# Optimization experiments

Hardware: AMD Instinct MI355X
Metric: run time of the kernel (lower is better)

## Reference

```python
import jax, jax.numpy as jnp
import numpy as np

B, N, DIM = 8, 1024, 1024
HEADS, DIM_HEAD = 16, 64
INNER = HEADS * DIM_HEAD  # 1024


def setup_inputs() -> dict:
    key = jax.random.key(0)
    k1, k2, k3 = jax.random.split(key, 3)
    x = jax.random.normal(k1, (B, N, DIM), dtype=jnp.float32)
    # Dense kernels (Glorot-ish scale for numerical sanity)
    w_qkv = jax.random.normal(k2, (DIM, 3 * INNER), dtype=jnp.float32) * (DIM ** -0.5)
    w_out = jax.random.normal(k3, (INNER, DIM), dtype=jnp.float32) * (INNER ** -0.5)
    b_out = jnp.zeros((DIM,), dtype=jnp.float32)
    return {"x": x, "w_qkv": w_qkv, "w_out": w_out, "b_out": b_out}


def reference(x, w_qkv, w_out, b_out):
    scale = DIM_HEAD ** -0.5
    qkv = x @ w_qkv                                   # [B, N, 3*INNER]
    q, k, v = jnp.split(qkv, 3, axis=-1)              # each [B, N, INNER]

    def to_heads(t):
        # [B, N, H*Dh] -> [B, H, N, Dh]
        return t.reshape(B, N, HEADS, DIM_HEAD).transpose(0, 2, 1, 3)

    q, k, v = to_heads(q), to_heads(k), to_heads(v)
    dots = jnp.einsum("bhid,bhjd->bhij", q, k) * scale   # [B, H, N, N]
    attn = jax.nn.softmax(dots, axis=-1)
    out = jnp.einsum("bhij,bhjd->bhid", attn, v)          # [B, H, N, Dh]
    out = out.transpose(0, 2, 1, 3).reshape(B, N, INNER)  # merge heads
    return out @ w_out + b_out                            # project_out (dropout inactive at inference)
```

## Files before the change

kernel.cpp:

```cpp
#include <hip/hip_runtime.h>
#include <hip/hip_bf16.h>
#include <math.h>

typedef __bf16 bf16_t;
typedef __bf16 bf16x4 __attribute__((ext_vector_type(4)));
typedef __bf16 bf16x8 __attribute__((ext_vector_type(8)));
typedef float f32x4 __attribute__((ext_vector_type(4)));

#define LOG2E 1.44269504088896340736f

#define GL2LDS(g, l)                                                     \
  __builtin_amdgcn_global_load_lds(                                      \
      (const __attribute__((address_space(1))) unsigned int*)(g),        \
      (__attribute__((address_space(3))) unsigned int*)(l), 16, 0, 0)

__global__ __launch_bounds__(256) void convert_f32_bf16(const float* __restrict__ in,
                                                        bf16_t* __restrict__ out) {
  const size_t idx = (size_t)(blockIdx.x * 256 + threadIdx.x) * 8;
  f32x4 a = *(const f32x4*)&in[idx];
  f32x4 b = *(const f32x4*)&in[idx + 4];
  bf16x8 v;
#pragma unroll
  for (int i = 0; i < 4; i++) { v[i] = (bf16_t)a[i]; v[i + 4] = (bf16_t)b[i]; }
  *(bf16x8*)&out[idx] = v;
}

__global__ __launch_bounds__(256) void transpose_f32_bf16(const float* __restrict__ in,
                                                          bf16_t* __restrict__ out,
                                                          int R, int C) {
  __shared__ bf16_t t[64][65];
  const int c0 = blockIdx.x * 64, r0 = blockIdx.y * 64;
  const int tx = threadIdx.x, ty = threadIdx.y;
#pragma unroll
  for (int i = 0; i < 16; i++) {
    int r = ty + i * 4;
    t[r][tx] = (bf16_t)in[(size_t)(r0 + r) * C + c0 + tx];
  }
  __syncthreads();
#pragma unroll
  for (int i = 0; i < 16; i++) {
    int r = ty + i * 4;
    out[(size_t)(c0 + r) * R + r0 + tx] = t[tx][r];
  }
}

template <int MODE>
__global__ __launch_bounds__(256) void gemm128(const bf16_t* __restrict__ A,
                                               const bf16_t* __restrict__ Bt,
                                               bf16_t* __restrict__ Qb,
                                               bf16_t* __restrict__ Kb,
                                               bf16_t* __restrict__ Vtb,
                                               const float* __restrict__ bias,
                                               float* __restrict__ Out) {
  constexpr int K = 1024;
  __shared__ __align__(16) bf16_t As[128 * 64];
  __shared__ __align__(16) bf16_t Bs[128 * 64];
  const int m0 = blockIdx.y * 128, n0 = blockIdx.x * 128;
  const int tid = threadIdx.x;
  const int w = tid >> 6, l = tid & 63;
  const int lr = l & 15, lq = l >> 4;
  const int lrx = lr & 7;
  const int wm = (w & 1) * 64, wn = (w >> 1) * 64;
  const int sR[4] = {(0 * 256 + tid) >> 3, (1 * 256 + tid) >> 3,
                     (2 * 256 + tid) >> 3, (3 * 256 + tid) >> 3};
  int sC[4];
#pragma unroll
  for (int i = 0; i < 4; i++) sC[i] = ((tid & 7) ^ (sR[i] & 7)) * 8;
  f32x4 acc[4][4] = {};

  for (int k0 = 0; k0 < K; k0 += 64) {
#pragma unroll
    for (int i = 0; i < 4; i++) {
      const int ldsoff = (i * 256 + w * 64) * 8;
      GL2LDS(&A[(size_t)(m0 + sR[i]) * K + k0 + sC[i]], &As[ldsoff]);
      GL2LDS(&Bt[(size_t)(n0 + sR[i]) * K + k0 + sC[i]], &Bs[ldsoff]);
    }
    __syncthreads();
#pragma unroll
    for (int ks = 0; ks < 2; ks++) {
      const int g = ks * 4 + lq;
      const int sw = ((g ^ lrx) << 3);
      bf16x8 af[4], bfr[4];
#pragma unroll
      for (int mt = 0; mt < 4; mt++)
        af[mt] = *(const bf16x8*)&As[((wm + mt * 16 + lr) << 6) + sw];
#pragma unroll
      for (int nt = 0; nt < 4; nt++)
        bfr[nt] = *(const bf16x8*)&Bs[((wn + nt * 16 + lr) << 6) + sw];
#pragma unroll
      for (int mt = 0; mt < 4; mt++)
#pragma unroll
        for (int nt = 0; nt < 4; nt++)
          acc[mt][nt] = __builtin_amdgcn_mfma_f32_16x16x32_bf16(af[mt], bfr[nt],
                                                                acc[mt][nt], 0, 0, 0);
    }
    __syncthreads();
  }

#pragma unroll
  for (int mt = 0; mt < 4; mt++)
#pragma unroll
    for (int nt = 0; nt < 4; nt++)
#pragma unroll
      for (int i = 0; i < 4; i++) {
        int m = m0 + wm + mt * 16 + lq * 4 + i;
        int c = n0 + wn + nt * 16 + lr;
        float v = acc[mt][nt][i];
        if (MODE == 1) {
          Out[(size_t)m * 1024 + c] = v + bias[c];
        } else {
          int b = m >> 10, n = m & 1023;
          int which = c >> 10, cc = c & 1023;
          int hh = cc >> 6, d = cc & 63;
          size_t qk = ((size_t)((b * 16 + hh) * 1024 + n)) * 64 + d;
          if (which == 0)
            Qb[qk] = (bf16_t)(v * (0.125f * LOG2E));
          else if (which == 1)
            Kb[qk] = (bf16_t)v;
          else
            Vtb[((size_t)((b * 16 + hh) * 64 + d)) * 1024 + n] = (bf16_t)v;
        }
      }
}

#define KVS 68
#define PS  72
__global__ __launch_bounds__(256) void attn128(const bf16_t* __restrict__ Qb,
                                               const bf16_t* __restrict__ Kb,
                                               const bf16_t* __restrict__ Vtb,
                                               bf16_t* __restrict__ Ob) {
  __shared__ __align__(16) bf16_t Ks[2][64 * KVS];
  __shared__ __align__(16) bf16_t Vs[2][64 * KVS];
  __shared__ __align__(16) bf16_t Pl[4 * 32 * PS];
  const int bid = blockIdx.x;
  const int qt = bid & 7, h = (bid >> 3) & 15, b = bid >> 7;
  const bf16_t* Qh = Qb + (size_t)((b * 16 + h) * 1024) * 64;
  const bf16_t* Kh = Kb + (size_t)((b * 16 + h) * 1024) * 64;
  const bf16_t* Vh = Vtb + (size_t)((b * 16 + h) * 64) * 1024;
  const int tid = threadIdx.x, w = tid >> 6, l = tid & 63;
  const int lr = l & 15, lq = l >> 4;
  const int q0 = qt * 128 + w * 32;

  bf16x8 onesf;
#pragma unroll
  for (int i = 0; i < 8; i++) onesf[i] = (lr == 0) ? (bf16_t)1.0f : (bf16_t)0.0f;

  const int sr = tid >> 3, sc = tid & 7;

  bf16x8 qf[2][2];
#pragma unroll
  for (int mt = 0; mt < 2; mt++)
#pragma unroll
    for (int ks = 0; ks < 2; ks++)
      qf[mt][ks] = *(const bf16x8*)&Qh[(size_t)(q0 + mt * 16 + lr) * 64 + ks * 32 + lq * 8];

  {
    bf16x8 k0 = *(const bf16x8*)&Kh[(size_t)sr * 64 + sc * 8];
    bf16x8 k1 = *(const bf16x8*)&Kh[(size_t)(sr + 32) * 64 + sc * 8];
    bf16x8 v0 = *(const bf16x8*)&Vh[(size_t)sr * 1024 + sc * 8];
    bf16x8 v1 = *(const bf16x8*)&Vh[(size_t)(sr + 32) * 1024 + sc * 8];
    *(bf16x8*)&Ks[0][sr * KVS + sc * 8] = k0;
    *(bf16x8*)&Ks[0][(sr + 32) * KVS + sc * 8] = k1;
    *(bf16x8*)&Vs[0][sr * KVS + sc * 8] = v0;
    *(bf16x8*)&Vs[0][(sr + 32) * KVS + sc * 8] = v1;
  }
  __syncthreads();

  f32x4 o[2][4] = {};
  f32x4 o5[2] = {};
  bf16_t* pw = &Pl[w * 32 * PS];

  for (int it = 0; it < 16; ++it) {
    const int buf = it & 1;
    bf16x8 nk0, nk1, nv0, nv1;
    if (it < 15) {
      const int jn = (it + 1) * 64;
      nk0 = *(const bf16x8*)&Kh[(size_t)(jn + sr) * 64 + sc * 8];
      nk1 = *(const bf16x8*)&Kh[(size_t)(jn + sr + 32) * 64 + sc * 8];
      nv0 = *(const bf16x8*)&Vh[(size_t)sr * 1024 + jn + sc * 8];
      nv1 = *(const bf16x8*)&Vh[(size_t)(sr + 32) * 1024 + jn + sc * 8];
    }
    f32x4 s[2][4] = {};
#pragma unroll
    for (int ks = 0; ks < 2; ks++)
#pragma unroll
      for (int nt = 0; nt < 4; nt++) {
        bf16x8 kf = *(const bf16x8*)&Ks[buf][(nt * 16 + lr) * KVS + ks * 32 + lq * 8];
#pragma unroll
        for (int mt = 0; mt < 2; mt++)
          s[mt][nt] = __builtin_amdgcn_mfma_f32_16x16x32_bf16(qf[mt][ks], kf, s[mt][nt], 0, 0, 0);
      }
#pragma unroll
    for (int mt = 0; mt < 2; mt++)
#pragma unroll
      for (int nt = 0; nt < 4; nt++)
#pragma unroll
        for (int i = 0; i < 4; i++)
          pw[(mt * 16 + lq * 4 + i) * PS + nt * 16 + lr] = (bf16_t)exp2f(s[mt][nt][i]);
#pragma unroll
    for (int ks = 0; ks < 2; ks++) {
      bf16x8 af[2];
#pragma unroll
      for (int mt = 0; mt < 2; mt++)
        af[mt] = *(const bf16x8*)&pw[(mt * 16 + lr) * PS + ks * 32 + lq * 8];
#pragma unroll
      for (int nt = 0; nt < 4; nt++) {
        bf16x8 vf = *(const bf16x8*)&Vs[buf][(nt * 16 + lr) * KVS + ks * 32 + lq * 8];
#pragma unroll
        for (int mt = 0; mt < 2; mt++)
          o[mt][nt] = __builtin_amdgcn_mfma_f32_16x16x32_bf16(af[mt], vf, o[mt][nt], 0, 0, 0);
      }
#pragma unroll
      for (int mt = 0; mt < 2; mt++)
        o5[mt] = __builtin_amdgcn_mfma_f32_16x16x32_bf16(af[mt], onesf, o5[mt], 0, 0, 0);
    }
    if (it < 15) {
      *(bf16x8*)&Ks[buf ^ 1][sr * KVS + sc * 8] = nk0;
      *(bf16x8*)&Ks[buf ^ 1][(sr + 32) * KVS + sc * 8] = nk1;
      *(bf16x8*)&Vs[buf ^ 1][sr * KVS + sc * 8] = nv0;
      *(bf16x8*)&Vs[buf ^ 1][(sr + 32) * KVS + sc * 8] = nv1;
    }
    __syncthreads();
  }
#pragma unroll
  for (int mt = 0; mt < 2; mt++)
#pragma unroll
    for (int i = 0; i < 4; i++) {
      float lsum = __shfl(o5[mt][i], lq * 16);
      float inv = 1.0f / lsum;
      int grow = b * 1024 + q0 + mt * 16 + lq * 4 + i;
#pragma unroll
      for (int nt = 0; nt < 4; nt++) {
        int col = h * 64 + nt * 16 + lr;
        Ob[(size_t)grow * 1024 + col] = (bf16_t)(o[mt][nt][i] * inv);
      }
    }
}

extern "C" void kernel_launch(void* const* d_in, const int* in_sizes, int n_in,
                              void* d_out, int out_size, void* d_ws, size_t ws_size,
                              hipStream_t stream) {
  const float* x     = (const float*)d_in[0];
  const float* w_qkv = (const float*)d_in[1];
  const float* w_out = (const float*)d_in[2];
  const float* b_out = (const float*)d_in[3];
  float* out = (float*)d_out;

  bf16_t* ws = (bf16_t*)d_ws;
  const size_t SZ = (size_t)8 * 1024 * 1024;
  bf16_t* Qb  = ws;
  bf16_t* Kb  = Qb + SZ;
  bf16_t* Vtb = Kb + SZ;
  bf16_t* Ob  = Vtb + SZ;
  bf16_t* Wqt = Ob + SZ;
  bf16_t* Wot = Wqt + (size_t)3072 * 1024;
  bf16_t* Xb  = Ob;

  hipLaunchKernelGGL(convert_f32_bf16, dim3(4096), dim3(256), 0, stream, x, Xb);
  hipLaunchKernelGGL(transpose_f32_bf16, dim3(48, 16), dim3(64, 4), 0, stream,
                     w_qkv, Wqt, 1024, 3072);
  hipLaunchKernelGGL(transpose_f32_bf16, dim3(16, 16), dim3(64, 4), 0, stream,
                     w_out, Wot, 1024, 1024);
  hipLaunchKernelGGL((gemm128<0>), dim3(24, 64), dim3(256), 0, stream,
                     Xb, Wqt, Qb, Kb, Vtb, (const float*)nullptr, (float*)nullptr);
  hipLaunchKernelGGL(attn128, dim3(1024), dim3(256), 0, stream, Qb, Kb, Vtb, Ob);
  hipLaunchKernelGGL((gemm128<1>), dim3(8, 64), dim3(256), 0, stream,
                     Ob, Wot, (bf16_t*)nullptr, (bf16_t*)nullptr, (bf16_t*)nullptr,
                     b_out, out);
}
```

Measured before the change: 282.2 us.

## Async direct-to-LDS K/V loads with XOR swizzle in attention; narrower out-proj tiles

The attention kernel now loads K and V tiles with global_load_lds straight into an XOR-swizzled unpadded LDS layout. This replaces the register staging and the separate LDS store phase, so the next tile's copy overlaps compute without holding registers. Block indexing is reordered so the query tile is the slowest-varying index, and the P scratch pitch changes. The output projection GEMM uses a 128x64 tile, doubling its grid to 1024 blocks for better CU occupancy, at the cost of less reuse per block.

After: 323.5 us. +14.6%, slower.

```diff
diff --git a/kernel.cpp b/kernel.cpp
--- a/kernel.cpp
+++ b/kernel.cpp
@@ -44,7 +44,7 @@
   }
 }
 
-template <int MODE>
+template <int MODE, int BN>
 __global__ __launch_bounds__(256) void gemm128(const bf16_t* __restrict__ A,
                                                const bf16_t* __restrict__ Bt,
                                                bf16_t* __restrict__ Qb,
@@ -53,26 +53,33 @@
                                                const float* __restrict__ bias,
                                                float* __restrict__ Out) {
   constexpr int K = 1024;
+  constexpr int NT = BN / 32;
+  constexpr int NB = BN / 32;
   __shared__ __align__(16) bf16_t As[128 * 64];
-  __shared__ __align__(16) bf16_t Bs[128 * 64];
-  const int m0 = blockIdx.y * 128, n0 = blockIdx.x * 128;
+  __shared__ __align__(16) bf16_t Bs[BN * 64];
+  const int m0 = blockIdx.y * 128, n0 = blockIdx.x * BN;
   const int tid = threadIdx.x;
   const int w = tid >> 6, l = tid & 63;
   const int lr = l & 15, lq = l >> 4;
   const int lrx = lr & 7;
-  const int wm = (w & 1) * 64, wn = (w >> 1) * 64;
-  const int sR[4] = {(0 * 256 + tid) >> 3, (1 * 256 + tid) >> 3,
-                     (2 * 256 + tid) >> 3, (3 * 256 + tid) >> 3};
-  int sC[4];
-#pragma unroll
-  for (int i = 0; i < 4; i++) sC[i] = ((tid & 7) ^ (sR[i] & 7)) * 8;
-  f32x4 acc[4][4] = {};
+  const int wm = (w & 1) * 64, wn = (w >> 1) * (BN / 2);
+  int sR[4], sC[4];
+#pragma unroll
+  for (int i = 0; i < 4; i++) {
+    sR[i] = (i * 256 + tid) >> 3;
+    sC[i] = ((tid & 7) ^ (sR[i] & 7)) * 8;
+  }
+  f32x4 acc[4][NT] = {};
 
   for (int k0 = 0; k0 < K; k0 += 64) {
 #pragma unroll
     for (int i = 0; i < 4; i++) {
       const int ldsoff = (i * 256 + w * 64) * 8;
       GL2LDS(&A[(size_t)(m0 + sR[i]) * K + k0 + sC[i]], &As[ldsoff]);
+    }
+#pragma unroll
+    for (int i = 0; i < NB; i++) {
+      const int ldsoff = (i * 256 + w * 64) * 8;
       GL2LDS(&Bt[(size_t)(n0 + sR[i]) * K + k0 + sC[i]], &Bs[ldsoff]);
     }
     __syncthreads();
@@ -80,17 +87,17 @@
     for (int ks = 0; ks < 2; ks++) {
       const int g = ks * 4 + lq;
       const int sw = ((g ^ lrx) << 3);
-      bf16x8 af[4], bfr[4];
+      bf16x8 af[4], bfr[NT];
 #pragma unroll
       for (int mt = 0; mt < 4; mt++)
         af[mt] = *(const bf16x8*)&As[((wm + mt * 16 + lr) << 6) + sw];
 #pragma unroll
-      for (int nt = 0; nt < 4; nt++)
+      for (int nt = 0; nt < NT; nt++)
         bfr[nt] = *(const bf16x8*)&Bs[((wn + nt * 16 + lr) << 6) + sw];
 #pragma unroll
       for (int mt = 0; mt < 4; mt++)
 #pragma unroll
-        for (int nt = 0; nt < 4; nt++)
+        for (int nt = 0; nt < NT; nt++)
           acc[mt][nt] = __builtin_amdgcn_mfma_f32_16x16x32_bf16(af[mt], bfr[nt],
                                                                 acc[mt][nt], 0, 0, 0);
     }
@@ -100,7 +107,7 @@
 #pragma unroll
   for (int mt = 0; mt < 4; mt++)
 #pragma unroll
-    for (int nt = 0; nt < 4; nt++)
+    for (int nt = 0; nt < NT; nt++)
 #pragma unroll
       for (int i = 0; i < 4; i++) {
         int m = m0 + wm + mt * 16 + lq * 4 + i;
@@ -123,29 +130,33 @@
       }
 }
 
-#define KVS 68
-#define PS  72
+#define PS 76
 __global__ __launch_bounds__(256) void attn128(const bf16_t* __restrict__ Qb,
                                                const bf16_t* __restrict__ Kb,
                                                const bf16_t* __restrict__ Vtb,
                                                bf16_t* __restrict__ Ob) {
-  __shared__ __align__(16) bf16_t Ks[2][64 * KVS];
-  __shared__ __align__(16) bf16_t Vs[2][64 * KVS];
+  __shared__ __align__(16) bf16_t Ks[2][64 * 64];
+  __shared__ __align__(16) bf16_t Vs[2][64 * 64];
   __shared__ __align__(16) bf16_t Pl[4 * 32 * PS];
   const int bid = blockIdx.x;
-  const int qt = bid & 7, h = (bid >> 3) & 15, b = bid >> 7;
+  const int qt = bid >> 7, idx = bid & 127;
+  const int h = idx & 15, b = idx >> 4;
   const bf16_t* Qh = Qb + (size_t)((b * 16 + h) * 1024) * 64;
   const bf16_t* Kh = Kb + (size_t)((b * 16 + h) * 1024) * 64;
   const bf16_t* Vh = Vtb + (size_t)((b * 16 + h) * 64) * 1024;
   const int tid = threadIdx.x, w = tid >> 6, l = tid & 63;
   const int lr = l & 15, lq = l >> 4;
+  const int lrx = lr & 7;
   const int q0 = qt * 128 + w * 32;
 
   bf16x8 onesf;
 #pragma unroll
   for (int i = 0; i < 8; i++) onesf[i] = (lr == 0) ? (bf16_t)1.0f : (bf16_t)0.0f;
 
-  const int sr = tid >> 3, sc = tid & 7;
+  const int sr = tid >> 3;
+  const int scc = ((tid & 7) ^ (sr & 7)) * 8;
+  const int ldsA = w * 512;
+  const int ldsB = 2048 + w * 512;
 
   bf16x8 qf[2][2];
 #pragma unroll
@@ -154,16 +165,10 @@
     for (int ks = 0; ks < 2; ks++)
       qf[mt][ks] = *(const bf16x8*)&Qh[(size_t)(q0 + mt * 16 + lr) * 64 + ks * 32 + lq * 8];
 
-  {
-    bf16x8 k0 = *(const bf16x8*)&Kh[(size_t)sr * 64 + sc * 8];
-    bf16x8 k1 = *(const bf16x8*)&Kh[(size_t)(sr + 32) * 64 + sc * 8];
-    bf16x8 v0 = *(const bf16x8*)&Vh[(size_t)sr * 1024 + sc * 8];
-    bf16x8 v1 = *(const bf16x8*)&Vh[(size_t)(sr + 32) * 1024 + sc * 8];
-    *(bf16x8*)&Ks[0][sr * KVS + sc * 8] = k0;
-    *(bf16x8*)&Ks[0][(sr + 32) * KVS + sc * 8] = k1;
-    *(bf16x8*)&Vs[0][sr * KVS + sc * 8] = v0;
-    *(bf16x8*)&Vs[0][(sr + 32) * KVS + sc * 8] = v1;
-  }
+  GL2LDS(&Kh[(size_t)sr * 64 + scc], &Ks[0][ldsA]);
+  GL2LDS(&Kh[(size_t)(sr + 32) * 64 + scc], &Ks[0][ldsB]);
+  GL2LDS(&Vh[(size_t)sr * 1024 + scc], &Vs[0][ldsA]);
+  GL2LDS(&Vh[(size_t)(sr + 32) * 1024 + scc], &Vs[0][ldsB]);
   __syncthreads();
 
   f32x4 o[2][4] = {};
@@ -172,24 +177,25 @@
 
   for (int it = 0; it < 16; ++it) {
     const int buf = it & 1;
-    bf16x8 nk0, nk1, nv0, nv1;
     if (it < 15) {
       const int jn = (it + 1) * 64;
-      nk0 = *(const bf16x8*)&Kh[(size_t)(jn + sr) * 64 + sc * 8];
-      nk1 = *(const bf16x8*)&Kh[(size_t)(jn + sr + 32) * 64 + sc * 8];
-      nv0 = *(const bf16x8*)&Vh[(size_t)sr * 1024 + jn + sc * 8];
-      nv1 = *(const bf16x8*)&Vh[(size_t)(sr + 32) * 1024 + jn + sc * 8];
+      GL2LDS(&Kh[(size_t)(jn + sr) * 64 + scc], &Ks[buf ^ 1][ldsA]);
+      GL2LDS(&Kh[(size_t)(jn + sr + 32) * 64 + scc], &Ks[buf ^ 1][ldsB]);
+      GL2LDS(&Vh[(size_t)sr * 1024 + jn + scc], &Vs[buf ^ 1][ldsA]);
+      GL2LDS(&Vh[(size_t)(sr + 32) * 1024 + jn + scc], &Vs[buf ^ 1][ldsB]);
     }
     f32x4 s[2][4] = {};
 #pragma unroll
-    for (int ks = 0; ks < 2; ks++)
+    for (int ks = 0; ks < 2; ks++) {
+      const int sw = (((ks * 4 + lq) ^ lrx) << 3);
 #pragma unroll
       for (int nt = 0; nt < 4; nt++) {
-        bf16x8 kf = *(const bf16x8*)&Ks[buf][(nt * 16 + lr) * KVS + ks * 32 + lq * 8];
+        bf16x8 kf = *(const bf16x8*)&Ks[buf][((nt * 16 + lr) << 6) + sw];
 #pragma unroll
         for (int mt = 0; mt < 2; mt++)
           s[mt][nt] = __builtin_amdgcn_mfma_f32_16x16x32_bf16(qf[mt][ks], kf, s[mt][nt], 0, 0, 0);
       }
+    }
 #pragma unroll
     for (int mt = 0; mt < 2; mt++)
 #pragma unroll
@@ -199,13 +205,14 @@
           pw[(mt * 16 + lq * 4 + i) * PS + nt * 16 + lr] = (bf16_t)exp2f(s[mt][nt][i]);
 #pragma unroll
     for (int ks = 0; ks < 2; ks++) {
+      const int sw = (((ks * 4 + lq) ^ lrx) << 3);
       bf16x8 af[2];
 #pragma unroll
       for (int mt = 0; mt < 2; mt++)
         af[mt] = *(const bf16x8*)&pw[(mt * 16 + lr) * PS + ks * 32 + lq * 8];
 #pragma unroll
       for (int nt = 0; nt < 4; nt++) {
-        bf16x8 vf = *(const bf16x8*)&Vs[buf][(nt * 16 + lr) * KVS + ks * 32 + lq * 8];
+        bf16x8 vf = *(const bf16x8*)&Vs[buf][((nt * 16 + lr) << 6) + sw];
 #pragma unroll
         for (int mt = 0; mt < 2; mt++)
           o[mt][nt] = __builtin_amdgcn_mfma_f32_16x16x32_bf16(af[mt], vf, o[mt][nt], 0, 0, 0);
@@ -213,12 +220,6 @@
 #pragma unroll
       for (int mt = 0; mt < 2; mt++)
         o5[mt] = __builtin_amdgcn_mfma_f32_16x16x32_bf16(af[mt], onesf, o5[mt], 0, 0, 0);
-    }
-    if (it < 15) {
-      *(bf16x8*)&Ks[buf ^ 1][sr * KVS + sc * 8] = nk0;
-      *(bf16x8*)&Ks[buf ^ 1][(sr + 32) * KVS + sc * 8] = nk1;
-      *(bf16x8*)&Vs[buf ^ 1][sr * KVS + sc * 8] = nv0;
-      *(bf16x8*)&Vs[buf ^ 1][(sr + 32) * KVS + sc * 8] = nv1;
     }
     __syncthreads();
   }
@@ -261,10 +262,10 @@
                      w_qkv, Wqt, 1024, 3072);
   hipLaunchKernelGGL(transpose_f32_bf16, dim3(16, 16), dim3(64, 4), 0, stream,
                      w_out, Wot, 1024, 1024);
-  hipLaunchKernelGGL((gemm128<0>), dim3(24, 64), dim3(256), 0, stream,
+  hipLaunchKernelGGL((gemm128<0, 128>), dim3(24, 64), dim3(256), 0, stream,
                      Xb, Wqt, Qb, Kb, Vtb, (const float*)nullptr, (float*)nullptr);
   hipLaunchKernelGGL(attn128, dim3(1024), dim3(256), 0, stream, Qb, Kb, Vtb, Ob);
-  hipLaunchKernelGGL((gemm128<1>), dim3(8, 64), dim3(256), 0, stream,
+  hipLaunchKernelGGL((gemm128<1, 64>), dim3(16, 64), dim3(256), 0, stream,
                      Ob, Wot, (bf16_t*)nullptr, (bf16_t*)nullptr, (bf16_t*)nullptr,
                      b_out, out);
 }
```
